# Performance work log

Measured on AMD Instinct MI355X. Metric: run time of the kernel, lower is better.

## Reference

```python
import jax, jax.numpy as jnp
import numpy as np

B, T1, T2 = 16, 2048, 2048
C_IN, C_HID, C_OUT = 1024, 1024, 1024


def setup_inputs() -> dict:
    key = jax.random.key(0)
    ks = jax.random.split(key, 8)
    q = jax.random.normal(ks[0], (B, T1, C_IN), dtype=jnp.float32)
    k = jax.random.normal(ks[1], (B, T2, C_IN), dtype=jnp.float32)
    v = jax.random.normal(ks[2], (B, T2, C_IN), dtype=jnp.float32)
    mask = jnp.ones((B, T1, T2), dtype=jnp.bool_)
    s_in = 1.0 / np.sqrt(C_IN)
    s_hid = 1.0 / np.sqrt(C_HID)
    Wq = jax.random.uniform(ks[3], (C_HID, C_IN), jnp.float32, -s_in, s_in)
    bq = jax.random.uniform(ks[4], (C_HID,), jnp.float32, -s_in, s_in)
    # fc_keys is initialized as a clone of fc_query in the torch module
    Wk = Wq.copy()
    bk = bq.copy()
    Wv = jax.random.uniform(ks[5], (C_HID, C_IN), jnp.float32, -s_in, s_in)
    bv = jax.random.uniform(ks[6], (C_HID,), jnp.float32, -s_in, s_in)
    Wo = jax.random.uniform(ks[7], (C_OUT, C_HID), jnp.float32, -s_hid, s_hid)
    bo = jnp.zeros((C_OUT,), dtype=jnp.float32)
    return {"q": q, "k": k, "v": v, "mask": mask,
            "Wq": Wq, "bq": bq, "Wk": Wk, "bk": bk,
            "Wv": Wv, "bv": bv, "Wo": Wo, "bo": bo}


def reference(q, k, v, mask, Wq, bq, Wk, bk, Wv, bv, Wo, bo):
    # 1x1 Conv1d over (batch, time, channels) == linear projection per timestep
    qp = jnp.einsum('btc,hc->bth', q, Wq) + bq  # (B, T1, H)
    kp = jnp.einsum('btc,hc->bth', k, Wk) + bk  # (B, T2, H)
    vp = jnp.einsum('btc,hc->bth', v, Wv) + bv  # (B, T2, H)
    scores = jnp.einsum('bqh,bkh->bqk', qp, kp)  # (B, T1, T2); no scaling in original
    scores = jnp.where(mask, scores, -jnp.inf)
    weights = jax.nn.softmax(scores, axis=-1)
    align = jnp.einsum('bqk,bkh->bqh', weights, vp)  # (B, T1, H)
    out = jnp.einsum('bth,oh->bto', align, Wo) + bo  # (B, T1, C_OUT)
    return (out, weights)
```

## Files before the change

kernel.cpp:

```cpp
#include <hip/hip_runtime.h>


typedef __bf16 bf16;
typedef __attribute__((ext_vector_type(8))) __bf16 bf16x8;
typedef __attribute__((ext_vector_type(4))) __bf16 bf16x4v;
typedef __attribute__((ext_vector_type(4))) float f32x4;

constexpr int BM = 128, BN = 128, BK = 32;

__device__ __forceinline__ f32x4 mfma_bf16(bf16x8 a, bf16x8 b, f32x4 c) {
  return __builtin_amdgcn_mfma_f32_16x16x32_bf16(a, b, c, 0, 0, 0);
}

__device__ __forceinline__ void async_ld16(const bf16* g, bf16* l) {
  __builtin_amdgcn_global_load_lds((const void*)g, (void*)l, 16, 0, 0);
}

__global__ void conv_split_k(const float4* __restrict__ x, bf16x4v* __restrict__ hi,
                             bf16x4v* __restrict__ lo, int n4) {
  int i = blockIdx.x * 256 + threadIdx.x;
  if (i >= n4) return;
  float4 v = x[i];
  float a[4] = {v.x, v.y, v.z, v.w};
  bf16x4v h, l;
#pragma unroll
  for (int c = 0; c < 4; c++) {
    bf16 hh = (bf16)a[c];
    h[c] = hh;
    l[c] = (bf16)(a[c] - (float)hh);
  }
  hi[i] = h;
  lo[i] = l;
}

__global__ void conv_plain_k(const float4* __restrict__ x, bf16x4v* __restrict__ hi, int n4) {
  int i = blockIdx.x * 256 + threadIdx.x;
  if (i >= n4) return;
  float4 v = x[i];
  float a[4] = {v.x, v.y, v.z, v.w};
  bf16x4v h;
#pragma unroll
  for (int c = 0; c < 4; c++) h[c] = (bf16)a[c];
  hi[i] = h;
}

__global__ __launch_bounds__(256, 3) void gemm_plain(
    const bf16* __restrict__ A, const bf16* __restrict__ Bm,
    const float* __restrict__ bias, float* __restrict__ outF, bf16* __restrict__ outB,
    int M, int N, int K, long aBatch, long bBatch, int storeMode) {
  __shared__ alignas(16) bf16 As[BM * BK];
  __shared__ alignas(16) bf16 Bs[BN * BK];
  const int tid = threadIdx.x;
  const int lane = tid & 63;
  const int wave = tid >> 6;
  const int wm = (wave >> 1) * 64;
  const int wn = (wave & 1) * 64;
  const long bm = (long)blockIdx.y * BM;
  const long bn = (long)blockIdx.x * BN;
  const int z = blockIdx.z;
  const bf16* Ab = A + (long)z * aBatch + bm * K;
  const bf16* Bb = Bm + (long)z * bBatch + bn * K;
  const int sr = tid >> 2;
  const int sc = (tid & 3) * 8;
  const int fr = lane & 15;
  const int kq = (lane >> 4) * 8;
  f32x4 acc[4][4] = {};
  for (int k0 = 0; k0 < K; k0 += BK) {
    async_ld16(Ab + (long)sr * K + k0 + sc, As + sr * BK + sc);
    async_ld16(Ab + (long)(sr + 64) * K + k0 + sc, As + (sr + 64) * BK + sc);
    async_ld16(Bb + (long)sr * K + k0 + sc, Bs + sr * BK + sc);
    async_ld16(Bb + (long)(sr + 64) * K + k0 + sc, Bs + (sr + 64) * BK + sc);
    __builtin_amdgcn_s_waitcnt(0);
    __syncthreads();
    bf16x8 af[4], bg[4];
#pragma unroll
    for (int i = 0; i < 4; i++)
      af[i] = *(const bf16x8*)(As + (wm + i * 16 + fr) * BK + kq);
#pragma unroll
    for (int j = 0; j < 4; j++)
      bg[j] = *(const bf16x8*)(Bs + (wn + j * 16 + fr) * BK + kq);
#pragma unroll
    for (int i = 0; i < 4; i++)
#pragma unroll
      for (int j = 0; j < 4; j++)
        acc[i][j] = mfma_bf16(af[i], bg[j], acc[i][j]);
    __syncthreads();
  }
  const int q4 = (lane >> 4) * 4;
  const long rowZ = (long)z * M;
#pragma unroll
  for (int i = 0; i < 4; i++) {
#pragma unroll
    for (int j = 0; j < 4; j++) {
      const int cg = (int)bn + wn + j * 16 + fr;
      const float bb = bias ? bias[cg] : 0.0f;
#pragma unroll
      for (int rr = 0; rr < 4; rr++) {
        const long rg = rowZ + bm + wm + i * 16 + q4 + rr;
        const float val = acc[i][j][rr] + bb;
        if (storeMode == 0) {
          outF[rg * N + cg] = val;
        } else if (storeMode == 1) {
          outB[((rg >> 11) * 1024L + cg) * 2048L + (rg & 2047)] = (bf16)val;
        } else {
          outB[rg * N + cg] = (bf16)val;
        }
      }
    }
  }
}

__global__ __launch_bounds__(256, 2) void gemm_split(
    const bf16* __restrict__ Ah, const bf16* __restrict__ Al,
    const bf16* __restrict__ Bh, const bf16* __restrict__ Bl,
    const float* __restrict__ bias, float* __restrict__ outF,
    bf16* __restrict__ outHi, bf16* __restrict__ outLo,
    int M, int N, int K, long aBatch, long bBatch, int storeMode) {
  __shared__ alignas(16) bf16 Ahs[BM * BK];
  __shared__ alignas(16) bf16 Als[BM * BK];
  __shared__ alignas(16) bf16 Bhs[BN * BK];
  __shared__ alignas(16) bf16 Bls[BN * BK];
  const int tid = threadIdx.x;
  const int lane = tid & 63;
  const int wave = tid >> 6;
  const int wm = (wave >> 1) * 64;
  const int wn = (wave & 1) * 64;
  const long bm = (long)blockIdx.y * BM;
  const long bn = (long)blockIdx.x * BN;
  const int z = blockIdx.z;
  const bf16* Ahb = Ah + (long)z * aBatch + bm * K;
  const bf16* Alb = Al + (long)z * aBatch + bm * K;
  const bf16* Bhb = Bh + (long)z * bBatch + bn * K;
  const bf16* Blb = Bl + (long)z * bBatch + bn * K;
  const int sr = tid >> 2;
  const int sc = (tid & 3) * 8;
  const int fr = lane & 15;
  const int kq = (lane >> 4) * 8;
  f32x4 acc[4][4] = {};
  for (int k0 = 0; k0 < K; k0 += BK) {
    async_ld16(Ahb + (long)sr * K + k0 + sc, Ahs + sr * BK + sc);
    async_ld16(Ahb + (long)(sr + 64) * K + k0 + sc, Ahs + (sr + 64) * BK + sc);
    async_ld16(Alb + (long)sr * K + k0 + sc, Als + sr * BK + sc);
    async_ld16(Alb + (long)(sr + 64) * K + k0 + sc, Als + (sr + 64) * BK + sc);
    async_ld16(Bhb + (long)sr * K + k0 + sc, Bhs + sr * BK + sc);
    async_ld16(Bhb + (long)(sr + 64) * K + k0 + sc, Bhs + (sr + 64) * BK + sc);
    async_ld16(Blb + (long)sr * K + k0 + sc, Bls + sr * BK + sc);
    async_ld16(Blb + (long)(sr + 64) * K + k0 + sc, Bls + (sr + 64) * BK + sc);
    __builtin_amdgcn_s_waitcnt(0);
    __syncthreads();
    bf16x8 ah[4], al[4], bh[4], bl[4];
#pragma unroll
    for (int i = 0; i < 4; i++) {
      ah[i] = *(const bf16x8*)(Ahs + (wm + i * 16 + fr) * BK + kq);
      al[i] = *(const bf16x8*)(Als + (wm + i * 16 + fr) * BK + kq);
    }
#pragma unroll
    for (int j = 0; j < 4; j++) {
      bh[j] = *(const bf16x8*)(Bhs + (wn + j * 16 + fr) * BK + kq);
      bl[j] = *(const bf16x8*)(Bls + (wn + j * 16 + fr) * BK + kq);
    }
#pragma unroll
    for (int i = 0; i < 4; i++)
#pragma unroll
      for (int j = 0; j < 4; j++) {
        acc[i][j] = mfma_bf16(ah[i], bh[j], acc[i][j]);
        acc[i][j] = mfma_bf16(ah[i], bl[j], acc[i][j]);
        acc[i][j] = mfma_bf16(al[i], bh[j], acc[i][j]);
      }
    __syncthreads();
  }
  const int q4 = (lane >> 4) * 4;
  const long rowZ = (long)z * M;
#pragma unroll
  for (int i = 0; i < 4; i++) {
#pragma unroll
    for (int j = 0; j < 4; j++) {
      const int cg = (int)bn + wn + j * 16 + fr;
      const float bb = bias ? bias[cg] : 0.0f;
#pragma unroll
      for (int rr = 0; rr < 4; rr++) {
        const long rg = rowZ + bm + wm + i * 16 + q4 + rr;
        const float val = acc[i][j][rr] + bb;
        if (storeMode == 0) {
          outF[rg * N + cg] = val;
        } else {
          const bf16 h = (bf16)val;
          outHi[rg * N + cg] = h;
          outLo[rg * N + cg] = (bf16)(val - (float)h);
        }
      }
    }
  }
}

__global__ __launch_bounds__(256) void softmax_rows(float* __restrict__ sc, bf16* __restrict__ wb) {
  const long row = blockIdx.x;
  float* p = sc + row * 2048;
  bf16* w = wb + row * 2048;
  const int tid = threadIdx.x;
  const int lane = tid & 63;
  const int wave = tid >> 6;
  float4 x0 = reinterpret_cast<float4*>(p)[tid];
  float4 x1 = reinterpret_cast<float4*>(p)[tid + 256];
  float m = fmaxf(fmaxf(fmaxf(x0.x, x0.y), fmaxf(x0.z, x0.w)),
                  fmaxf(fmaxf(x1.x, x1.y), fmaxf(x1.z, x1.w)));
#pragma unroll
  for (int off = 32; off > 0; off >>= 1) m = fmaxf(m, __shfl_xor(m, off));
  __shared__ float sm[4], ssum[4];
  if (lane == 0) sm[wave] = m;
  __syncthreads();
  m = fmaxf(fmaxf(sm[0], sm[1]), fmaxf(sm[2], sm[3]));
  float e0 = __expf(x0.x - m), e1 = __expf(x0.y - m), e2 = __expf(x0.z - m), e3 = __expf(x0.w - m);
  float e4 = __expf(x1.x - m), e5 = __expf(x1.y - m), e6 = __expf(x1.z - m), e7 = __expf(x1.w - m);
  float s = ((e0 + e1) + (e2 + e3)) + ((e4 + e5) + (e6 + e7));
#pragma unroll
  for (int off = 32; off > 0; off >>= 1) s += __shfl_xor(s, off);
  if (lane == 0) ssum[wave] = s;
  __syncthreads();
  s = (ssum[0] + ssum[1]) + (ssum[2] + ssum[3]);
  const float inv = 1.0f / s;
  float4 y0 = make_float4(e0 * inv, e1 * inv, e2 * inv, e3 * inv);
  float4 y1 = make_float4(e4 * inv, e5 * inv, e6 * inv, e7 * inv);
  reinterpret_cast<float4*>(p)[tid] = y0;
  reinterpret_cast<float4*>(p)[tid + 256] = y1;
  bf16x4v b0, b1;
  b0[0] = (bf16)y0.x; b0[1] = (bf16)y0.y; b0[2] = (bf16)y0.z; b0[3] = (bf16)y0.w;
  b1[0] = (bf16)y1.x; b1[1] = (bf16)y1.y; b1[2] = (bf16)y1.z; b1[3] = (bf16)y1.w;
  reinterpret_cast<bf16x4v*>(w)[tid] = b0;
  reinterpret_cast<bf16x4v*>(w)[tid + 256] = b1;
}

extern "C" void kernel_launch(void* const* d_in, const int* in_sizes, int n_in,
                              void* d_out, int out_size, void* d_ws, size_t ws_size,
                              hipStream_t stream) {
  (void)in_sizes; (void)n_in; (void)out_size; (void)ws_size;
  const float* q  = (const float*)d_in[0];
  const float* k  = (const float*)d_in[1];
  const float* v  = (const float*)d_in[2];
  const float* Wq = (const float*)d_in[4];
  const float* bq = (const float*)d_in[5];
  const float* Wk = (const float*)d_in[6];
  const float* bk = (const float*)d_in[7];
  const float* Wv = (const float*)d_in[8];
  const float* bv = (const float*)d_in[9];
  const float* Wo = (const float*)d_in[10];
  const float* bo = (const float*)d_in[11];

  constexpr int NQ = 16 * 2048 * 1024;
  constexpr int NW = 1024 * 1024;

  float* outp   = (float*)d_out;
  float* scores = outp + NQ;
  bf16* qp_h = (bf16*)d_out;
  bf16* qp_l = qp_h + NQ;

  char* ws = (char*)d_ws;
  const size_t MB = (size_t)1 << 20;
  bf16* X    = (bf16*)(ws);
  bf16* Xlo  = (bf16*)(ws + 64 * MB);
  bf16* vpT  = (bf16*)(ws + 128 * MB);
  bf16* kp_h = (bf16*)(ws + 192 * MB);
  bf16* kp_l = (bf16*)(ws + 256 * MB);
  bf16* Wq_h = (bf16*)(ws + 320 * MB);
  bf16* Wq_l = (bf16*)(ws + 322 * MB);
  bf16* Wk_h = (bf16*)(ws + 324 * MB);
  bf16* Wk_l = (bf16*)(ws + 326 * MB);
  bf16* Wv_h = (bf16*)(ws + 328 * MB);
  bf16* Wo_h = (bf16*)(ws + 330 * MB);
  bf16* v_h  = kp_h;
  bf16* w_bf = X;
  bf16* alig = kp_h;

  conv_split_k<<<NW / 1024, 256, 0, stream>>>((const float4*)Wq, (bf16x4v*)Wq_h, (bf16x4v*)Wq_l, NW / 4);
  conv_split_k<<<NW / 1024, 256, 0, stream>>>((const float4*)Wk, (bf16x4v*)Wk_h, (bf16x4v*)Wk_l, NW / 4);
  conv_plain_k<<<NW / 1024, 256, 0, stream>>>((const float4*)Wv, (bf16x4v*)Wv_h, NW / 4);
  conv_plain_k<<<NW / 1024, 256, 0, stream>>>((const float4*)Wo, (bf16x4v*)Wo_h, NW / 4);

  conv_plain_k<<<NQ / 1024, 256, 0, stream>>>((const float4*)v, (bf16x4v*)v_h, NQ / 4);
  gemm_plain<<<dim3(8, 256, 1), 256, 0, stream>>>(v_h, Wv_h, bv, nullptr, vpT,
                                                  32768, 1024, 1024, 0, 0, 1);

  conv_split_k<<<NQ / 1024, 256, 0, stream>>>((const float4*)q, (bf16x4v*)X, (bf16x4v*)Xlo, NQ / 4);
  gemm_split<<<dim3(8, 256, 1), 256, 0, stream>>>(X, Xlo, Wq_h, Wq_l, bq, nullptr, qp_h, qp_l,
                                                  32768, 1024, 1024, 0, 0, 1);

  conv_split_k<<<NQ / 1024, 256, 0, stream>>>((const float4*)k, (bf16x4v*)X, (bf16x4v*)Xlo, NQ / 4);
  gemm_split<<<dim3(8, 256, 1), 256, 0, stream>>>(X, Xlo, Wk_h, Wk_l, bk, nullptr, kp_h, kp_l,
                                                  32768, 1024, 1024, 0, 0, 1);

  gemm_split<<<dim3(16, 16, 16), 256, 0, stream>>>(qp_h, qp_l, kp_h, kp_l, nullptr, scores,
                                                   nullptr, nullptr,
                                                   2048, 2048, 1024, 2048L * 1024L, 2048L * 1024L, 0);

  softmax_rows<<<32768, 256, 0, stream>>>(scores, w_bf);

  gemm_plain<<<dim3(8, 16, 16), 256, 0, stream>>>(w_bf, vpT, nullptr, nullptr, alig,
                                                  2048, 1024, 2048, 2048L * 2048L, 1024L * 2048L, 2);

  gemm_plain<<<dim3(8, 256, 1), 256, 0, stream>>>(alig, Wo_h, bo, outp, nullptr,
                                                  32768, 1024, 1024, 0, 0, 0);
}
```

Baseline: 2.160 ms.

## Fold query and key projections into precomputed Wq^T·Wk matrix

Precomputes M = Wq^T·Wk and the vector Wk^T·bq, computes q·M with split-bf16 GEMM, and feeds raw k directly into the scores GEMM with a per-key bias column. Terms constant per query row are dropped since softmax is shift-invariant. This removes the full key projection GEMM and its hi/lo intermediates, at the cost of different rounding and pre-softmax scores that differ by a row-constant.

```diff
diff --git a/kernel.cpp b/kernel.cpp
--- a/kernel.cpp
+++ b/kernel.cpp
@@ -17,20 +17,35 @@
 }
 
 __global__ void conv_split_k(const float4* __restrict__ x, bf16x4v* __restrict__ hi,
-                             bf16x4v* __restrict__ lo, int n4) {
-  int i = blockIdx.x * 256 + threadIdx.x;
-  if (i >= n4) return;
-  float4 v = x[i];
-  float a[4] = {v.x, v.y, v.z, v.w};
-  bf16x4v h, l;
-#pragma unroll
-  for (int c = 0; c < 4; c++) {
-    bf16 hh = (bf16)a[c];
-    h[c] = hh;
-    l[c] = (bf16)(a[c] - (float)hh);
-  }
-  hi[i] = h;
-  lo[i] = l;
+                             bf16x4v* __restrict__ lo, int n4,
+                             const float4* __restrict__ beta, float* __restrict__ rowOut) {
+  const int i = blockIdx.x * 256 + threadIdx.x;
+  float dot = 0.0f;
+  if (i < n4) {
+    float4 v = x[i];
+    float a[4] = {v.x, v.y, v.z, v.w};
+    bf16x4v h, l;
+#pragma unroll
+    for (int c = 0; c < 4; c++) {
+      bf16 hh = (bf16)a[c];
+      h[c] = hh;
+      l[c] = (bf16)(a[c] - (float)hh);
+    }
+    hi[i] = h;
+    lo[i] = l;
+    if (beta) {
+      float4 b = beta[threadIdx.x];
+      dot = v.x * b.x + v.y * b.y + v.z * b.z + v.w * b.w;
+    }
+  }
+  if (rowOut) {
+#pragma unroll
+    for (int off = 32; off > 0; off >>= 1) dot += __shfl_xor(dot, off);
+    __shared__ float sred[4];
+    if ((threadIdx.x & 63) == 0) sred[threadIdx.x >> 6] = dot;
+    __syncthreads();
+    if (threadIdx.x == 0) rowOut[blockIdx.x] = (sred[0] + sred[1]) + (sred[2] + sred[3]);
+  }
 }
 
 __global__ void conv_plain_k(const float4* __restrict__ x, bf16x4v* __restrict__ hi, int n4) {
@@ -42,6 +57,35 @@
 #pragma unroll
   for (int c = 0; c < 4; c++) h[c] = (bf16)a[c];
   hi[i] = h;
+}
+
+__global__ void conv_split_T(const float* __restrict__ W, bf16* __restrict__ th,
+                             bf16* __restrict__ tl) {
+  const int c = blockIdx.x * 256 + threadIdx.x;
+  const int h0 = blockIdx.y * 4;
+  bf16x4v hh, ll;
+#pragma unroll
+  for (int j = 0; j < 4; j++) {
+    float w = W[(long)(h0 + j) * 1024 + c];
+    bf16 hi = (bf16)w;
+    hh[j] = hi;
+    ll[j] = (bf16)(w - (float)hi);
+  }
+  *(bf16x4v*)(th + (long)c * 1024 + h0) = hh;
+  *(bf16x4v*)(tl + (long)c * 1024 + h0) = ll;
+}
+
+__global__ void col_gemv(const float* __restrict__ W, const float* __restrict__ b,
+                         float* __restrict__ out) {
+  __shared__ float bs[1024];
+  const int tid = threadIdx.x;
+#pragma unroll
+  for (int j = 0; j < 4; j++) bs[tid + 256 * j] = b[tid + 256 * j];
+  __syncthreads();
+  const int c = blockIdx.x * 256 + tid;
+  float s = 0.0f;
+  for (int h = 0; h < 1024; h++) s += W[(long)h * 1024 + c] * bs[h];
+  out[c] = s;
 }
 
 __global__ __launch_bounds__(256, 3) void gemm_plain(
@@ -113,8 +157,8 @@
 __global__ __launch_bounds__(256, 2) void gemm_split(
     const bf16* __restrict__ Ah, const bf16* __restrict__ Al,
     const bf16* __restrict__ Bh, const bf16* __restrict__ Bl,
-    const float* __restrict__ bias, float* __restrict__ outF,
-    bf16* __restrict__ outHi, bf16* __restrict__ outLo,
+    const float* __restrict__ bias, const float* __restrict__ colAdd,
+    float* __restrict__ outF, bf16* __restrict__ outHi, bf16* __restrict__ outLo,
     int M, int N, int K, long aBatch, long bBatch, int storeMode) {
   __shared__ alignas(16) bf16 Ahs[BM * BK];
   __shared__ alignas(16) bf16 Als[BM * BK];
@@ -177,10 +221,11 @@
     for (int j = 0; j < 4; j++) {
       const int cg = (int)bn + wn + j * 16 + fr;
       const float bb = bias ? bias[cg] : 0.0f;
+      const float ca = colAdd ? colAdd[(long)z * N + cg] : 0.0f;
 #pragma unroll
       for (int rr = 0; rr < 4; rr++) {
         const long rg = rowZ + bm + wm + i * 16 + q4 + rr;
-        const float val = acc[i][j][rr] + bb;
+        const float val = acc[i][j][rr] + bb + ca;
         if (storeMode == 0) {
           outF[rg * N + cg] = val;
         } else {
@@ -240,7 +285,6 @@
   const float* Wq = (const float*)d_in[4];
   const float* bq = (const float*)d_in[5];
   const float* Wk = (const float*)d_in[6];
-  const float* bk = (const float*)d_in[7];
   const float* Wv = (const float*)d_in[8];
   const float* bv = (const float*)d_in[9];
   const float* Wo = (const float*)d_in[10];
@@ -251,8 +295,8 @@
 
   float* outp   = (float*)d_out;
   float* scores = outp + NQ;
-  bf16* qp_h = (bf16*)d_out;
-  bf16* qp_l = qp_h + NQ;
+  bf16* t1_h = (bf16*)d_out;
+  bf16* t1_l = t1_h + NQ;
 
   char* ws = (char*)d_ws;
   const size_t MB = (size_t)1 << 20;
@@ -260,36 +304,45 @@
   bf16* Xlo  = (bf16*)(ws + 64 * MB);
   bf16* vpT  = (bf16*)(ws + 128 * MB);
   bf16* kp_h = (bf16*)(ws + 192 * MB);
-  bf16* kp_l = (bf16*)(ws + 256 * MB);
-  bf16* Wq_h = (bf16*)(ws + 320 * MB);
-  bf16* Wq_l = (bf16*)(ws + 322 * MB);
-  bf16* Wk_h = (bf16*)(ws + 324 * MB);
-  bf16* Wk_l = (bf16*)(ws + 326 * MB);
+  bf16* MT_h = (bf16*)(ws + 256 * MB);
+  bf16* MT_l = (bf16*)(ws + 258 * MB);
+  float* beta = (float*)(ws + 260 * MB);
+  float* krow = (float*)(ws + 261 * MB);
+  bf16* QT_h = (bf16*)(ws + 320 * MB);
+  bf16* QT_l = (bf16*)(ws + 322 * MB);
+  bf16* KT_h = (bf16*)(ws + 324 * MB);
+  bf16* KT_l = (bf16*)(ws + 326 * MB);
   bf16* Wv_h = (bf16*)(ws + 328 * MB);
   bf16* Wo_h = (bf16*)(ws + 330 * MB);
   bf16* v_h  = kp_h;
   bf16* w_bf = X;
   bf16* alig = kp_h;
 
-  conv_split_k<<<NW / 1024, 256, 0, stream>>>((const float4*)Wq, (bf16x4v*)Wq_h, (bf16x4v*)Wq_l, NW / 4);
-  conv_split_k<<<NW / 1024, 256, 0, stream>>>((const float4*)Wk, (bf16x4v*)Wk_h, (bf16x4v*)Wk_l, NW / 4);
+  conv_split_T<<<dim3(4, 256, 1), 256, 0, stream>>>(Wq, QT_h, QT_l);
+  conv_split_T<<<dim3(4, 256, 1), 256, 0, stream>>>(Wk, KT_h, KT_l);
+  col_gemv<<<4, 256, 0, stream>>>(Wk, bq, beta);
   conv_plain_k<<<NW / 1024, 256, 0, stream>>>((const float4*)Wv, (bf16x4v*)Wv_h, NW / 4);
   conv_plain_k<<<NW / 1024, 256, 0, stream>>>((const float4*)Wo, (bf16x4v*)Wo_h, NW / 4);
+
+  gemm_split<<<dim3(8, 8, 1), 256, 0, stream>>>(KT_h, KT_l, QT_h, QT_l, nullptr, nullptr,
+                                                nullptr, MT_h, MT_l,
+                                                1024, 1024, 1024, 0, 0, 1);
 
   conv_plain_k<<<NQ / 1024, 256, 0, stream>>>((const float4*)v, (bf16x4v*)v_h, NQ / 4);
   gemm_plain<<<dim3(8, 256, 1), 256, 0, stream>>>(v_h, Wv_h, bv, nullptr, vpT,
                                                   32768, 1024, 1024, 0, 0, 1);
 
-  conv_split_k<<<NQ / 1024, 256, 0, stream>>>((const float4*)q, (bf16x4v*)X, (bf16x4v*)Xlo, NQ / 4);
-  gemm_split<<<dim3(8, 256, 1), 256, 0, stream>>>(X, Xlo, Wq_h, Wq_l, bq, nullptr, qp_h, qp_l,
+  conv_split_k<<<NQ / 1024, 256, 0, stream>>>((const float4*)q, (bf16x4v*)X, (bf16x4v*)Xlo,
+                                              NQ / 4, nullptr, nullptr);
+  gemm_split<<<dim3(8, 256, 1), 256, 0, stream>>>(X, Xlo, MT_h, MT_l, nullptr, nullptr,
+                                                  nullptr, t1_h, t1_l,
                                                   32768, 1024, 1024, 0, 0, 1);
 
-  conv_split_k<<<NQ / 1024, 256, 0, stream>>>((const float4*)k, (bf16x4v*)X, (bf16x4v*)Xlo, NQ / 4);
-  gemm_split<<<dim3(8, 256, 1), 256, 0, stream>>>(X, Xlo, Wk_h, Wk_l, bk, nullptr, kp_h, kp_l,
-                                                  32768, 1024, 1024, 0, 0, 1);
-
-  gemm_split<<<dim3(16, 16, 16), 256, 0, stream>>>(qp_h, qp_l, kp_h, kp_l, nullptr, scores,
-                                                   nullptr, nullptr,
+  conv_split_k<<<NQ / 1024, 256, 0, stream>>>((const float4*)k, (bf16x4v*)X, (bf16x4v*)Xlo,
+                                              NQ / 4, (const float4*)beta, krow);
+
+  gemm_split<<<dim3(16, 16, 16), 256, 0, stream>>>(t1_h, t1_l, X, Xlo, nullptr, krow,
+                                                   scores, nullptr, nullptr,
                                                    2048, 2048, 1024, 2048L * 1024L, 2048L * 1024L, 0);
 
   softmax_rows<<<32768, 256, 0, stream>>>(scores, w_bf);
```

Measured after the change: 2.025 ms. 6.3% less time.
